# Kernel optimization log

Hardware: AMD Instinct MI355X
Metric: run time of the kernel (lower is better)

The kernel has to match this reference:

```python
import jax, jax.numpy as jnp
import numpy as np

N = 16_777_216  # number of draft tokens / cache slots
ACCEPT_PROB = 0.7


def setup_inputs() -> dict:
    key = jax.random.key(0)
    k1, k2, k3 = jax.random.split(key, 3)
    idx = jax.random.randint(k1, (N,), 0, N, dtype=jnp.int64)
    keep = jax.random.uniform(k2, (N,)) < ACCEPT_PROB
    # rejected slots are marked -1, as in the original kernel
    accept_index = jnp.where(keep, idx, jnp.int64(-1))
    out_cache_loc = jax.random.normal(k3, (N,), dtype=jnp.float32)
    return {"accept_index": accept_index, "out_cache_loc": out_cache_loc}


def reference(accept_index, out_cache_loc):
    """Stream compaction: gather out_cache_loc[accept_index[i]] for every i with
    accept_index[i] >= 0, packed densely at the front of the output.

    The original returns an array of length num_accepted (data-dependent). For a
    static, jit-compatible shape we return a length-N array whose first
    num_accepted entries equal the original output and the rest are zero.
    """
    n = accept_index.shape[0]
    mask = accept_index >= 0                      # [N] bool
    # exclusive prefix sum of mask = destination slot for each accepted element
    dst = jnp.cumsum(mask.astype(jnp.int64)) - mask.astype(jnp.int64)  # [N]
    # gather (use 0 as a safe dummy index for rejected lanes)
    vals = out_cache_loc[jnp.where(mask, accept_index, 0)]             # [N]
    # scatter accepted values to their compacted slots; rejected lanes are
    # routed to index n, which mode='drop' discards
    scatter_idx = jnp.where(mask, dst, n)
    out = jnp.zeros((n,), dtype=out_cache_loc.dtype)
    out = out.at[scatter_idx].set(vals, mode="drop")
    return out
```

## Files before the change

kernel.cpp:

```cpp
#include <hip/hip_runtime.h>


#define N_TOTAL  16777216
#define BLOCK    256

#define EPT2     16
#define TILE2    (BLOCK * EPT2)
#define NB2      (N_TOTAL / TILE2)
#define GRID     2048
#define GENS     (NB2 / GRID)

#define SLICE_LG 20
#define SLICES   (N_TOTAL >> SLICE_LG)

typedef float vfloat4 __attribute__((ext_vector_type(4)));
typedef int   vint4   __attribute__((ext_vector_type(4)));

__global__ __launch_bounds__(256) void k_init(unsigned long long* __restrict__ state) {
    state[blockIdx.x * 256 + threadIdx.x] = 0ULL;
}

__global__ __launch_bounds__(BLOCK, 8) void k_compact(const int* __restrict__ idx,
                                                      const float* __restrict__ src,
                                                      float* __restrict__ out,
                                                      unsigned long long* __restrict__ state) {
    const int b = blockIdx.x;
    const int t = threadIdx.x;
    const int lane = t & 63, wave = t >> 6;

    __shared__ int wsum[BLOCK / 64], woff[BLOCK / 64], btotal;
    __shared__ long long sBase;
    __shared__ float vals[TILE2];

    for (int gen = 0; gen < GENS; ++gen) {
        const int tile = b + gen * GRID;

        const vint4* p = (const vint4*)(idx + (size_t)tile * TILE2 + (size_t)t * EPT2);
        int v[EPT2];
#pragma unroll
        for (int j = 0; j < EPT2 / 4; ++j) {
            vint4 q = __builtin_nontemporal_load(p + j);
            v[4 * j + 0] = q.x; v[4 * j + 1] = q.y;
            v[4 * j + 2] = q.z; v[4 * j + 3] = q.w;
        }
        int cnt = 0;
#pragma unroll
        for (int j = 0; j < EPT2; ++j) cnt += (v[j] >= 0);

        int x = cnt;
#pragma unroll
        for (int d = 1; d < 64; d <<= 1) {
            int y = __shfl_up(x, d);
            if (lane >= d) x += y;
        }
        if (lane == 63) wsum[wave] = x;
        __syncthreads();
        if (t == 0) {
            int s = 0;
#pragma unroll
            for (int w = 0; w < BLOCK / 64; ++w) { woff[w] = s; s += wsum[w]; }
            btotal = s;
            if (tile == 0) {
                __hip_atomic_store(&state[0], ((unsigned long long)s << 2) | 2ULL,
                                   __ATOMIC_RELAXED, __HIP_MEMORY_SCOPE_AGENT);
                sBase = 0;
            } else {
                __hip_atomic_store(&state[tile], ((unsigned long long)s << 2) | 1ULL,
                                   __ATOMIC_RELAXED, __HIP_MEMORY_SCOPE_AGENT);
            }
        }
        __syncthreads();

        const int off0 = (x - cnt) + woff[wave];

#pragma unroll 1
        for (int s = 0; s < SLICES; ++s) {
            float tmp[EPT2];
#pragma unroll
            for (int j = 0; j < EPT2; ++j) {
                const bool m = (int)((unsigned)v[j] >> SLICE_LG) == s;
                tmp[j] = src[m ? v[j] : 0];
            }
            asm volatile("s_waitcnt vmcnt(0)" ::: "memory");
            int o = off0;
#pragma unroll
            for (int j = 0; j < EPT2; ++j) {
                const bool acc = v[j] >= 0;
                const bool m = (int)((unsigned)v[j] >> SLICE_LG) == s;
                if (m) vals[o] = tmp[j];
                o += acc;
            }
        }

        if (tile > 0 && wave == 0) {
            long long excl = 0;
            int look = tile - 1;
            for (;;) {
                const int pos = look - lane;
                unsigned long long s = 2ULL;
                if (pos >= 0)
                    s = __hip_atomic_load(&state[pos], __ATOMIC_RELAXED,
                                          __HIP_MEMORY_SCOPE_AGENT);
                for (;;) {
                    const bool need = (pos >= 0) && ((s & 3ULL) == 0ULL);
                    if (!__any(need)) break;
                    if (need) {
                        __builtin_amdgcn_s_sleep(2);
                        s = __hip_atomic_load(&state[pos], __ATOMIC_RELAXED,
                                              __HIP_MEMORY_SCOPE_AGENT);
                    }
                }
                const unsigned long long ball = __ballot((s & 3ULL) == 2ULL);
                const int fp = ball ? (__ffsll((long long)ball) - 1) : 64;
                long long c = (lane <= fp) ? (long long)(s >> 2) : 0;
#pragma unroll
                for (int d = 32; d; d >>= 1) c += __shfl_down(c, d);
                excl += __shfl(c, 0);
                if (ball) break;
                look -= 64;
            }
            if (lane == 0) {
                __hip_atomic_store(&state[tile],
                                   (((unsigned long long)(excl + btotal)) << 2) | 2ULL,
                                   __ATOMIC_RELAXED, __HIP_MEMORY_SCOPE_AGENT);
                sBase = excl;
            }
        }
        __syncthreads();

        const int tot = btotal;
        const long long base = sBase;

        {
            const long long gbeg = base, gend = base + tot;
            const long long a0 = (gbeg + 3) & ~3LL;
            const long long a1 = gend & ~3LL;
            const long long hend = a0 < gend ? a0 : gend;
            for (long long g = gbeg + t; g < hend; g += BLOCK)
                __builtin_nontemporal_store(vals[(int)(g - gbeg)], out + g);
            if (a0 < gend) {
                for (long long g = a0 + (long long)t * 4; g < a1; g += (long long)BLOCK * 4) {
                    const int l = (int)(g - gbeg);
                    vfloat4 w = { vals[l], vals[l + 1], vals[l + 2], vals[l + 3] };
                    __builtin_nontemporal_store(w, (vfloat4*)(out + g));
                }
                for (long long g = a1 + t; g < gend; g += BLOCK)
                    __builtin_nontemporal_store(vals[(int)(g - gbeg)], out + g);
            }
        }

        {
            const long long rprev = (long long)tile * TILE2 - base;
            const int rcnt = TILE2 - tot;
            const long long zbeg = (long long)N_TOTAL - rprev - rcnt;
            const long long zend = (long long)N_TOTAL - rprev;
            const long long a0 = (zbeg + 3) & ~3LL;
            const long long a1 = zend & ~3LL;
            const long long hend = a0 < zend ? a0 : zend;
            for (long long g = zbeg + t; g < hend; g += BLOCK)
                __builtin_nontemporal_store(0.0f, out + g);
            if (a0 < zend) {
                const vfloat4 z = (vfloat4)(0.f);
                for (long long g = a0 + (long long)t * 4; g < a1; g += (long long)BLOCK * 4)
                    __builtin_nontemporal_store(z, (vfloat4*)(out + g));
                for (long long g = a1 + t; g < zend; g += BLOCK)
                    __builtin_nontemporal_store(0.0f, out + g);
            }
        }

        __syncthreads();
    }
}

extern "C" void kernel_launch(void* const* d_in, const int* in_sizes, int n_in,
                              void* d_out, int out_size, void* d_ws, size_t ws_size,
                              hipStream_t stream) {
    const int*   idx = (const int*)d_in[0];
    const float* src = (const float*)d_in[1];
    float*       out = (float*)d_out;

    unsigned long long* state = (unsigned long long*)d_ws;

    k_init   <<<NB2 / 256, 256, 0, stream>>>(state);
    k_compact<<<GRID, BLOCK, 0, stream>>>(idx, src, out, state);
}
```

Measured before the change: 328.3 us.

## Double-buffer sliced gathers and launch one block per tile

Drops the persistent generation loop: the kernel now launches one block per tile (NB2 blocks) and lowers the launch-bounds occupancy hint from 8 to 4. The per-slice gather is software-pipelined with two register buffers, so one slice's loads are issued before the previous slice is committed to LDS, waiting on vmcnt(16) instead of draining to zero. Gathers now use nontemporal loads, and masked-out lanes point at the start of the current slice instead of index 0. The aim is to hide gather latency and remove the per-generation barrier overhead. The cost is higher register pressure, possible loss of L2 reuse from the nontemporal hint, and a decoupled look-back that now relies on in-order block dispatch across many more blocks.

```diff
diff --git a/kernel.cpp b/kernel.cpp
--- a/kernel.cpp
+++ b/kernel.cpp
@@ -7,9 +7,6 @@
 #define EPT2     16
 #define TILE2    (BLOCK * EPT2)
 #define NB2      (N_TOTAL / TILE2)
-#define GRID     2048
-#define GENS     (NB2 / GRID)
-
 #define SLICE_LG 20
 #define SLICES   (N_TOTAL >> SLICE_LG)
 
@@ -20,7 +17,27 @@
     state[blockIdx.x * 256 + threadIdx.x] = 0ULL;
 }
 
-__global__ __launch_bounds__(BLOCK, 8) void k_compact(const int* __restrict__ idx,
+#define GATHER_ISSUE(sl, tmp)                                              \
+    _Pragma("unroll")                                                      \
+    for (int j = 0; j < EPT2; ++j) {                                       \
+        const bool m_ = (int)((unsigned)v[j] >> SLICE_LG) == (sl);         \
+        const int a_ = m_ ? v[j] : ((sl) << SLICE_LG);                     \
+        tmp[j] = __builtin_nontemporal_load(src + a_);                     \
+    }
+
+#define GATHER_COMMIT(sl, tmp)                                             \
+    {                                                                      \
+        int o_ = off0;                                                     \
+        _Pragma("unroll")                                                  \
+        for (int j = 0; j < EPT2; ++j) {                                   \
+            const bool acc_ = v[j] >= 0;                                   \
+            const bool m_ = (int)((unsigned)v[j] >> SLICE_LG) == (sl);     \
+            if (m_) vals[o_] = tmp[j];                                     \
+            o_ += acc_;                                                    \
+        }                                                                  \
+    }
+
+__global__ __launch_bounds__(BLOCK, 4) void k_compact(const int* __restrict__ idx,
                                                       const float* __restrict__ src,
                                                       float* __restrict__ out,
                                                       unsigned long long* __restrict__ state) {
@@ -32,143 +49,136 @@
     __shared__ long long sBase;
     __shared__ float vals[TILE2];
 
-    for (int gen = 0; gen < GENS; ++gen) {
-        const int tile = b + gen * GRID;
+    const vint4* p = (const vint4*)(idx + (size_t)b * TILE2 + (size_t)t * EPT2);
+    int v[EPT2];
+#pragma unroll
+    for (int j = 0; j < EPT2 / 4; ++j) {
+        vint4 q = __builtin_nontemporal_load(p + j);
+        v[4 * j + 0] = q.x; v[4 * j + 1] = q.y;
+        v[4 * j + 2] = q.z; v[4 * j + 3] = q.w;
+    }
+    int cnt = 0;
+#pragma unroll
+    for (int j = 0; j < EPT2; ++j) cnt += (v[j] >= 0);
 
-        const vint4* p = (const vint4*)(idx + (size_t)tile * TILE2 + (size_t)t * EPT2);
-        int v[EPT2];
+    int x = cnt;
 #pragma unroll
-        for (int j = 0; j < EPT2 / 4; ++j) {
-            vint4 q = __builtin_nontemporal_load(p + j);
-            v[4 * j + 0] = q.x; v[4 * j + 1] = q.y;
-            v[4 * j + 2] = q.z; v[4 * j + 3] = q.w;
+    for (int d = 1; d < 64; d <<= 1) {
+        int y = __shfl_up(x, d);
+        if (lane >= d) x += y;
+    }
+    if (lane == 63) wsum[wave] = x;
+    __syncthreads();
+    if (t == 0) {
+        int s = 0;
+#pragma unroll
+        for (int w = 0; w < BLOCK / 64; ++w) { woff[w] = s; s += wsum[w]; }
+        btotal = s;
+        if (b == 0) {
+            __hip_atomic_store(&state[0], ((unsigned long long)s << 2) | 2ULL,
+                               __ATOMIC_RELAXED, __HIP_MEMORY_SCOPE_AGENT);
+            sBase = 0;
+        } else {
+            __hip_atomic_store(&state[b], ((unsigned long long)s << 2) | 1ULL,
+                               __ATOMIC_RELAXED, __HIP_MEMORY_SCOPE_AGENT);
         }
-        int cnt = 0;
-#pragma unroll
-        for (int j = 0; j < EPT2; ++j) cnt += (v[j] >= 0);
+    }
+    __syncthreads();
 
-        int x = cnt;
-#pragma unroll
-        for (int d = 1; d < 64; d <<= 1) {
-            int y = __shfl_up(x, d);
-            if (lane >= d) x += y;
+    const int off0 = (x - cnt) + woff[wave];
+
+    {
+        float tA[EPT2], tB[EPT2];
+        GATHER_ISSUE(0, tA);
+#pragma unroll 1
+        for (int s = 0; s < SLICES; s += 2) {
+            GATHER_ISSUE(s + 1, tB);
+            asm volatile("s_waitcnt vmcnt(16)" ::: "memory");
+            GATHER_COMMIT(s, tA);
+            if (s + 2 < SLICES) {
+                GATHER_ISSUE(s + 2, tA);
+                asm volatile("s_waitcnt vmcnt(16)" ::: "memory");
+            } else {
+                asm volatile("s_waitcnt vmcnt(0)" ::: "memory");
+            }
+            GATHER_COMMIT(s + 1, tB);
         }
-        if (lane == 63) wsum[wave] = x;
-        __syncthreads();
-        if (t == 0) {
-            int s = 0;
-#pragma unroll
-            for (int w = 0; w < BLOCK / 64; ++w) { woff[w] = s; s += wsum[w]; }
-            btotal = s;
-            if (tile == 0) {
-                __hip_atomic_store(&state[0], ((unsigned long long)s << 2) | 2ULL,
-                                   __ATOMIC_RELAXED, __HIP_MEMORY_SCOPE_AGENT);
-                sBase = 0;
-            } else {
-                __hip_atomic_store(&state[tile], ((unsigned long long)s << 2) | 1ULL,
-                                   __ATOMIC_RELAXED, __HIP_MEMORY_SCOPE_AGENT);
-            }
-        }
-        __syncthreads();
+    }
 
-        const int off0 = (x - cnt) + woff[wave];
-
-#pragma unroll 1
-        for (int s = 0; s < SLICES; ++s) {
-            float tmp[EPT2];
-#pragma unroll
-            for (int j = 0; j < EPT2; ++j) {
-                const bool m = (int)((unsigned)v[j] >> SLICE_LG) == s;
-                tmp[j] = src[m ? v[j] : 0];
-            }
-            asm volatile("s_waitcnt vmcnt(0)" ::: "memory");
-            int o = off0;
-#pragma unroll
-            for (int j = 0; j < EPT2; ++j) {
-                const bool acc = v[j] >= 0;
-                const bool m = (int)((unsigned)v[j] >> SLICE_LG) == s;
-                if (m) vals[o] = tmp[j];
-                o += acc;
-            }
-        }
-
-        if (tile > 0 && wave == 0) {
-            long long excl = 0;
-            int look = tile - 1;
+    if (b > 0 && wave == 0) {
+        long long excl = 0;
+        int look = b - 1;
+        for (;;) {
+            const int pos = look - lane;
+            unsigned long long s = 2ULL;
+            if (pos >= 0)
+                s = __hip_atomic_load(&state[pos], __ATOMIC_RELAXED,
+                                      __HIP_MEMORY_SCOPE_AGENT);
             for (;;) {
-                const int pos = look - lane;
-                unsigned long long s = 2ULL;
-                if (pos >= 0)
+                const bool need = (pos >= 0) && ((s & 3ULL) == 0ULL);
+                if (!__any(need)) break;
+                if (need) {
+                    __builtin_amdgcn_s_sleep(2);
                     s = __hip_atomic_load(&state[pos], __ATOMIC_RELAXED,
                                           __HIP_MEMORY_SCOPE_AGENT);
-                for (;;) {
-                    const bool need = (pos >= 0) && ((s & 3ULL) == 0ULL);
-                    if (!__any(need)) break;
-                    if (need) {
-                        __builtin_amdgcn_s_sleep(2);
-                        s = __hip_atomic_load(&state[pos], __ATOMIC_RELAXED,
-                                              __HIP_MEMORY_SCOPE_AGENT);
-                    }
                 }
-                const unsigned long long ball = __ballot((s & 3ULL) == 2ULL);
-                const int fp = ball ? (__ffsll((long long)ball) - 1) : 64;
-                long long c = (lane <= fp) ? (long long)(s >> 2) : 0;
+            }
+            const unsigned long long ball = __ballot((s & 3ULL) == 2ULL);
+            const int fp = ball ? (__ffsll((long long)ball) - 1) : 64;
+            long long c = (lane <= fp) ? (long long)(s >> 2) : 0;
 #pragma unroll
-                for (int d = 32; d; d >>= 1) c += __shfl_down(c, d);
-                excl += __shfl(c, 0);
-                if (ball) break;
-                look -= 64;
+            for (int d = 32; d; d >>= 1) c += __shfl_down(c, d);
+            excl += __shfl(c, 0);
+            if (ball) break;
+            look -= 64;
+        }
+        if (lane == 0) {
+            __hip_atomic_store(&state[b],
+                               (((unsigned long long)(excl + btotal)) << 2) | 2ULL,
+                               __ATOMIC_RELAXED, __HIP_MEMORY_SCOPE_AGENT);
+            sBase = excl;
+        }
+    }
+    __syncthreads();
+
+    const int tot = btotal;
+    const long long base = sBase;
+
+    {
+        const long long gbeg = base, gend = base + tot;
+        const long long a0 = (gbeg + 3) & ~3LL;
+        const long long a1 = gend & ~3LL;
+        const long long hend = a0 < gend ? a0 : gend;
+        for (long long g = gbeg + t; g < hend; g += BLOCK)
+            __builtin_nontemporal_store(vals[(int)(g - gbeg)], out + g);
+        if (a0 < gend) {
+            for (long long g = a0 + (long long)t * 4; g < a1; g += (long long)BLOCK * 4) {
+                const int l = (int)(g - gbeg);
+                vfloat4 w = { vals[l], vals[l + 1], vals[l + 2], vals[l + 3] };
+                __builtin_nontemporal_store(w, (vfloat4*)(out + g));
             }
-            if (lane == 0) {
-                __hip_atomic_store(&state[tile],
-                                   (((unsigned long long)(excl + btotal)) << 2) | 2ULL,
-                                   __ATOMIC_RELAXED, __HIP_MEMORY_SCOPE_AGENT);
-                sBase = excl;
-            }
+            for (long long g = a1 + t; g < gend; g += BLOCK)
+                __builtin_nontemporal_store(vals[(int)(g - gbeg)], out + g);
         }
-        __syncthreads();
+    }
 
-        const int tot = btotal;
-        const long long base = sBase;
-
-        {
-            const long long gbeg = base, gend = base + tot;
-            const long long a0 = (gbeg + 3) & ~3LL;
-            const long long a1 = gend & ~3LL;
-            const long long hend = a0 < gend ? a0 : gend;
-            for (long long g = gbeg + t; g < hend; g += BLOCK)
-                __builtin_nontemporal_store(vals[(int)(g - gbeg)], out + g);
-            if (a0 < gend) {
-                for (long long g = a0 + (long long)t * 4; g < a1; g += (long long)BLOCK * 4) {
-                    const int l = (int)(g - gbeg);
-                    vfloat4 w = { vals[l], vals[l + 1], vals[l + 2], vals[l + 3] };
-                    __builtin_nontemporal_store(w, (vfloat4*)(out + g));
-                }
-                for (long long g = a1 + t; g < gend; g += BLOCK)
-                    __builtin_nontemporal_store(vals[(int)(g - gbeg)], out + g);
-            }
+    {
+        const long long rprev = (long long)b * TILE2 - base;
+        const int rcnt = TILE2 - tot;
+        const long long zbeg = (long long)N_TOTAL - rprev - rcnt;
+        const long long zend = (long long)N_TOTAL - rprev;
+        const long long a0 = (zbeg + 3) & ~3LL;
+        const long long a1 = zend & ~3LL;
+        const long long hend = a0 < zend ? a0 : zend;
+        for (long long g = zbeg + t; g < hend; g += BLOCK)
+            __builtin_nontemporal_store(0.0f, out + g);
+        if (a0 < zend) {
+            const vfloat4 z = (vfloat4)(0.f);
+            for (long long g = a0 + (long long)t * 4; g < a1; g += (long long)BLOCK * 4)
+                __builtin_nontemporal_store(z, (vfloat4*)(out + g));
+            for (long long g = a1 + t; g < zend; g += BLOCK)
+                __builtin_nontemporal_store(0.0f, out + g);
         }
-
-        {
-            const long long rprev = (long long)tile * TILE2 - base;
-            const int rcnt = TILE2 - tot;
-            const long long zbeg = (long long)N_TOTAL - rprev - rcnt;
-            const long long zend = (long long)N_TOTAL - rprev;
-            const long long a0 = (zbeg + 3) & ~3LL;
-            const long long a1 = zend & ~3LL;
-            const long long hend = a0 < zend ? a0 : zend;
-            for (long long g = zbeg + t; g < hend; g += BLOCK)
-                __builtin_nontemporal_store(0.0f, out + g);
-            if (a0 < zend) {
-                const vfloat4 z = (vfloat4)(0.f);
-                for (long long g = a0 + (long long)t * 4; g < a1; g += (long long)BLOCK * 4)
-                    __builtin_nontemporal_store(z, (vfloat4*)(out + g));
-                for (long long g = a1 + t; g < zend; g += BLOCK)
-                    __builtin_nontemporal_store(0.0f, out + g);
-            }
-        }
-
-        __syncthreads();
     }
 }
 
@@ -182,5 +192,5 @@
     unsigned long long* state = (unsigned long long*)d_ws;
 
     k_init   <<<NB2 / 256, 256, 0, stream>>>(state);
-    k_compact<<<GRID, BLOCK, 0, stream>>>(idx, src, out, state);
+    k_compact<<<NB2, BLOCK, 0, stream>>>(idx, src, out, state);
 }
```

Measured after the change: 447.0 us. 36.2% more time.

## Bin accepted indices by source region before gathering to improve cache locality

Applied to the files above, without the earlier changes.

Replaces the single-pass compaction, which swept all source slices per tile, with a multi-kernel pipeline. It histograms accepted indices into 64 source regions, scans the counts, and bins (destination, index) pairs by region into workspace. It then gathers per region with XCD-aware block mapping so each region's source stays cache-resident, and writes the output in 32K-element chunks staged through LDS. The aim is to remove the 16x redundant slice gather loads and the random-access misses, at the cost of extra workspace traffic (dst/val arrays written and read several times) and more kernel launches. A fallback path keeps the old single-kernel approach when the workspace is too small.

```diff
diff --git a/kernel.cpp b/kernel.cpp
--- a/kernel.cpp
+++ b/kernel.cpp
@@ -3,16 +3,29 @@
 
 #define N_TOTAL  16777216
 #define BLOCK    256
-
-#define EPT2     16
-#define TILE2    (BLOCK * EPT2)
-#define NB2      (N_TOTAL / TILE2)
-#define GRID     2048
-#define GENS     (NB2 / GRID)
+#define EPT      16
+#define TILE     (BLOCK * EPT)
+#define NB       (N_TOTAL / TILE)
+
+#define NR       64
+#define REG_LG   18
+#define CSTR     4100
+
+#define CHUNK_LG 15
+#define CHUNK    (1 << CHUNK_LG)
+#define NCH      (N_TOTAL / CHUNK)
 
 #define SLICE_LG 20
 #define SLICES   (N_TOTAL >> SLICE_LG)
 
+#define OFF_STATE 0ull
+#define OFF_DST   32768ull
+#define OFF_VAL   (OFF_DST + 4ull * N_TOTAL)
+#define OFF_BB    (OFF_VAL + 4ull * N_TOTAL)
+#define OFF_CNT   (OFF_BB + 16400ull)
+#define OFF_RB    (OFF_CNT + 4ull * NR * CSTR)
+#define WS_NEED   (OFF_RB + 4ull * (NR + 1))
+
 typedef float vfloat4 __attribute__((ext_vector_type(4)));
 typedef int   vint4   __attribute__((ext_vector_type(4)));
 
@@ -20,155 +33,471 @@
     state[blockIdx.x * 256 + threadIdx.x] = 0ULL;
 }
 
-__global__ __launch_bounds__(BLOCK, 8) void k_compact(const int* __restrict__ idx,
-                                                      const float* __restrict__ src,
-                                                      float* __restrict__ out,
-                                                      unsigned long long* __restrict__ state) {
+__global__ __launch_bounds__(BLOCK) void k_histA(const int* __restrict__ idx,
+                                                 unsigned long long* __restrict__ state,
+                                                 int* __restrict__ blockBase,
+                                                 int* __restrict__ cntArr) {
     const int b = blockIdx.x;
     const int t = threadIdx.x;
     const int lane = t & 63, wave = t >> 6;
 
+    __shared__ int hist[NR];
     __shared__ int wsum[BLOCK / 64], woff[BLOCK / 64], btotal;
     __shared__ long long sBase;
-    __shared__ float vals[TILE2];
-
-    for (int gen = 0; gen < GENS; ++gen) {
-        const int tile = b + gen * GRID;
-
-        const vint4* p = (const vint4*)(idx + (size_t)tile * TILE2 + (size_t)t * EPT2);
-        int v[EPT2];
-#pragma unroll
-        for (int j = 0; j < EPT2 / 4; ++j) {
-            vint4 q = __builtin_nontemporal_load(p + j);
-            v[4 * j + 0] = q.x; v[4 * j + 1] = q.y;
-            v[4 * j + 2] = q.z; v[4 * j + 3] = q.w;
-        }
-        int cnt = 0;
-#pragma unroll
-        for (int j = 0; j < EPT2; ++j) cnt += (v[j] >= 0);
-
-        int x = cnt;
-#pragma unroll
-        for (int d = 1; d < 64; d <<= 1) {
-            int y = __shfl_up(x, d);
-            if (lane >= d) x += y;
-        }
-        if (lane == 63) wsum[wave] = x;
-        __syncthreads();
-        if (t == 0) {
-            int s = 0;
-#pragma unroll
-            for (int w = 0; w < BLOCK / 64; ++w) { woff[w] = s; s += wsum[w]; }
-            btotal = s;
-            if (tile == 0) {
-                __hip_atomic_store(&state[0], ((unsigned long long)s << 2) | 2ULL,
-                                   __ATOMIC_RELAXED, __HIP_MEMORY_SCOPE_AGENT);
-                sBase = 0;
-            } else {
-                __hip_atomic_store(&state[tile], ((unsigned long long)s << 2) | 1ULL,
-                                   __ATOMIC_RELAXED, __HIP_MEMORY_SCOPE_AGENT);
-            }
-        }
-        __syncthreads();
-
-        const int off0 = (x - cnt) + woff[wave];
-
-#pragma unroll 1
-        for (int s = 0; s < SLICES; ++s) {
-            float tmp[EPT2];
-#pragma unroll
-            for (int j = 0; j < EPT2; ++j) {
-                const bool m = (int)((unsigned)v[j] >> SLICE_LG) == s;
-                tmp[j] = src[m ? v[j] : 0];
-            }
-            asm volatile("s_waitcnt vmcnt(0)" ::: "memory");
-            int o = off0;
-#pragma unroll
-            for (int j = 0; j < EPT2; ++j) {
-                const bool acc = v[j] >= 0;
-                const bool m = (int)((unsigned)v[j] >> SLICE_LG) == s;
-                if (m) vals[o] = tmp[j];
-                o += acc;
-            }
-        }
-
-        if (tile > 0 && wave == 0) {
-            long long excl = 0;
-            int look = tile - 1;
+    for (int r = t; r < NR; r += BLOCK) hist[r] = 0;
+
+    const vint4* p = (const vint4*)(idx + (size_t)b * TILE + (size_t)t * EPT);
+    int v[EPT];
+#pragma unroll
+    for (int j = 0; j < EPT / 4; ++j) {
+        vint4 q = __builtin_nontemporal_load(p + j);
+        v[4 * j + 0] = q.x; v[4 * j + 1] = q.y;
+        v[4 * j + 2] = q.z; v[4 * j + 3] = q.w;
+    }
+    int ca = 0;
+#pragma unroll
+    for (int j = 0; j < EPT; ++j) ca += (v[j] >= 0);
+
+    int x = ca;
+#pragma unroll
+    for (int d = 1; d < 64; d <<= 1) {
+        int y = __shfl_up(x, d);
+        if (lane >= d) x += y;
+    }
+    if (lane == 63) wsum[wave] = x;
+    __syncthreads();
+    if (t == 0) {
+        int s = 0;
+#pragma unroll
+        for (int w = 0; w < BLOCK / 64; ++w) { woff[w] = s; s += wsum[w]; }
+        btotal = s;
+        if (b == 0) {
+            __hip_atomic_store(&state[0], ((unsigned long long)s << 2) | 2ULL,
+                               __ATOMIC_RELAXED, __HIP_MEMORY_SCOPE_AGENT);
+            sBase = 0;
+        } else {
+            __hip_atomic_store(&state[b], ((unsigned long long)s << 2) | 1ULL,
+                               __ATOMIC_RELAXED, __HIP_MEMORY_SCOPE_AGENT);
+        }
+    }
+    __syncthreads();
+
+#pragma unroll
+    for (int j = 0; j < EPT; ++j)
+        if (v[j] >= 0) atomicAdd(&hist[v[j] >> REG_LG], 1);
+    __syncthreads();
+    if (t < NR) cntArr[t * CSTR + b] = hist[t];
+
+    if (b > 0 && wave == 0) {
+        long long excl = 0;
+        int look = b - 1;
+        for (;;) {
+            const int pos = look - lane;
+            unsigned long long s = 2ULL;
+            if (pos >= 0)
+                s = __hip_atomic_load(&state[pos], __ATOMIC_RELAXED,
+                                      __HIP_MEMORY_SCOPE_AGENT);
             for (;;) {
-                const int pos = look - lane;
-                unsigned long long s = 2ULL;
-                if (pos >= 0)
+                const bool need = (pos >= 0) && ((s & 3ULL) == 0ULL);
+                if (!__any(need)) break;
+                if (need) {
+                    __builtin_amdgcn_s_sleep(2);
                     s = __hip_atomic_load(&state[pos], __ATOMIC_RELAXED,
                                           __HIP_MEMORY_SCOPE_AGENT);
-                for (;;) {
-                    const bool need = (pos >= 0) && ((s & 3ULL) == 0ULL);
-                    if (!__any(need)) break;
-                    if (need) {
-                        __builtin_amdgcn_s_sleep(2);
-                        s = __hip_atomic_load(&state[pos], __ATOMIC_RELAXED,
-                                              __HIP_MEMORY_SCOPE_AGENT);
-                    }
                 }
-                const unsigned long long ball = __ballot((s & 3ULL) == 2ULL);
-                const int fp = ball ? (__ffsll((long long)ball) - 1) : 64;
-                long long c = (lane <= fp) ? (long long)(s >> 2) : 0;
-#pragma unroll
-                for (int d = 32; d; d >>= 1) c += __shfl_down(c, d);
-                excl += __shfl(c, 0);
-                if (ball) break;
-                look -= 64;
             }
-            if (lane == 0) {
-                __hip_atomic_store(&state[tile],
-                                   (((unsigned long long)(excl + btotal)) << 2) | 2ULL,
-                                   __ATOMIC_RELAXED, __HIP_MEMORY_SCOPE_AGENT);
-                sBase = excl;
+            const unsigned long long ball = __ballot((s & 3ULL) == 2ULL);
+            const int fp = ball ? (__ffsll((long long)ball) - 1) : 64;
+            long long c = (lane <= fp) ? (long long)(s >> 2) : 0;
+#pragma unroll
+            for (int d = 32; d; d >>= 1) c += __shfl_down(c, d);
+            excl += __shfl(c, 0);
+            if (ball) break;
+            look -= 64;
+        }
+        if (lane == 0) {
+            __hip_atomic_store(&state[b],
+                               (((unsigned long long)(excl + btotal)) << 2) | 2ULL,
+                               __ATOMIC_RELAXED, __HIP_MEMORY_SCOPE_AGENT);
+            sBase = excl;
+        }
+    }
+    __syncthreads();
+    if (t == 0) blockBase[b] = (int)(b == 0 ? 0 : sBase);
+}
+
+__global__ __launch_bounds__(256) void k_scan64(int* __restrict__ cntArr) {
+    const int r = blockIdx.x, t = threadIdx.x;
+    const int lane = t & 63, wave = t >> 6;
+    int* row = cntArr + r * CSTR;
+    int vals[16];
+    const vint4* p = (const vint4*)(row + t * 16);
+#pragma unroll
+    for (int j = 0; j < 4; ++j) {
+        vint4 q = p[j];
+        vals[4 * j + 0] = q.x; vals[4 * j + 1] = q.y;
+        vals[4 * j + 2] = q.z; vals[4 * j + 3] = q.w;
+    }
+    int tsum = 0;
+#pragma unroll
+    for (int j = 0; j < 16; ++j) tsum += vals[j];
+    int x = tsum;
+#pragma unroll
+    for (int d = 1; d < 64; d <<= 1) {
+        int y = __shfl_up(x, d);
+        if (lane >= d) x += y;
+    }
+    __shared__ int wsum[4], woff[4];
+    if (lane == 63) wsum[wave] = x;
+    __syncthreads();
+    if (t == 0) {
+        int s = 0;
+#pragma unroll
+        for (int w = 0; w < 4; ++w) { woff[w] = s; s += wsum[w]; }
+        row[4096] = s;
+    }
+    __syncthreads();
+    int run = (x - tsum) + woff[wave];
+#pragma unroll
+    for (int j = 0; j < 16; ++j) {
+        row[t * 16 + j] = run;
+        run += vals[j];
+    }
+}
+
+__global__ __launch_bounds__(64) void k_scan2(const int* __restrict__ cntArr,
+                                              int* __restrict__ regionBase,
+                                              int* __restrict__ blockBase) {
+    const int t = threadIdx.x;
+    int x = cntArr[t * CSTR + 4096];
+    int incl = x;
+#pragma unroll
+    for (int d = 1; d < 64; d <<= 1) {
+        int y = __shfl_up(incl, d);
+        if (t >= d) incl += y;
+    }
+    regionBase[t] = incl - x;
+    if (t == 63) { regionBase[64] = incl; blockBase[4096] = incl; }
+}
+
+__global__ __launch_bounds__(BLOCK) void k_binB(const int* __restrict__ idx,
+                                                const int* __restrict__ blockBase,
+                                                const int* __restrict__ cntArr,
+                                                const int* __restrict__ regionBase,
+                                                int* __restrict__ dstArr,
+                                                int* __restrict__ valArr) {
+    const int b = blockIdx.x;
+    const int t = threadIdx.x;
+    const int lane = t & 63, wave = t >> 6;
+
+    __shared__ int hist[NR], rscan[NR + 1], rcnt[NR], sG[NR];
+    __shared__ int ldsD[TILE], ldsV[TILE];
+    __shared__ int wsum[BLOCK / 64], woff[BLOCK / 64], btotal;
+    for (int r = t; r < NR; r += BLOCK) { hist[r] = 0; rcnt[r] = 0; }
+
+    const vint4* p = (const vint4*)(idx + (size_t)b * TILE + (size_t)t * EPT);
+    int v[EPT];
+#pragma unroll
+    for (int j = 0; j < EPT / 4; ++j) {
+        vint4 q = __builtin_nontemporal_load(p + j);
+        v[4 * j + 0] = q.x; v[4 * j + 1] = q.y;
+        v[4 * j + 2] = q.z; v[4 * j + 3] = q.w;
+    }
+    int ca = 0;
+#pragma unroll
+    for (int j = 0; j < EPT; ++j) ca += (v[j] >= 0);
+
+    int x = ca;
+#pragma unroll
+    for (int d = 1; d < 64; d <<= 1) {
+        int y = __shfl_up(x, d);
+        if (lane >= d) x += y;
+    }
+    if (lane == 63) wsum[wave] = x;
+    __syncthreads();
+    if (t == 0) {
+        int s = 0;
+#pragma unroll
+        for (int w = 0; w < BLOCK / 64; ++w) { woff[w] = s; s += wsum[w]; }
+        btotal = s;
+    }
+    __syncthreads();
+    const int off0 = (x - ca) + woff[wave];
+    const int base = blockBase[b];
+
+#pragma unroll
+    for (int j = 0; j < EPT; ++j)
+        if (v[j] >= 0) atomicAdd(&hist[v[j] >> REG_LG], 1);
+    __syncthreads();
+    if (t == 0) {
+        int s = 0;
+#pragma unroll
+        for (int r = 0; r < NR; ++r) { rscan[r] = s; s += hist[r]; }
+        rscan[NR] = s;
+    }
+    if (t < NR) sG[t] = regionBase[t] + cntArr[t * CSTR + b];
+    __syncthreads();
+
+    int o = off0;
+#pragma unroll
+    for (int j = 0; j < EPT; ++j) {
+        if (v[j] >= 0) {
+            const int r = v[j] >> REG_LG;
+            const int pos = rscan[r] + atomicAdd(&rcnt[r], 1);
+            ldsD[pos] = base + o;
+            ldsV[pos] = v[j];
+            ++o;
+        }
+    }
+    __syncthreads();
+
+    const int tot = btotal;
+    for (int i = t; i < tot; i += BLOCK) {
+        int loR = 0, hiR = NR;
+        while (hiR - loR > 1) {
+            const int mid = (loR + hiR) >> 1;
+            if (rscan[mid] <= i) loR = mid; else hiR = mid;
+        }
+        const int g = sG[loR] + (i - rscan[loR]);
+        dstArr[g] = ldsD[i];
+        valArr[g] = ldsV[i];
+    }
+}
+
+__global__ __launch_bounds__(BLOCK) void k_gather(const float* __restrict__ src,
+                                                  const int* __restrict__ cntArr,
+                                                  const int* __restrict__ regionBase,
+                                                  int* __restrict__ valArr) {
+    const int b = blockIdx.x, t = threadIdx.x;
+    const int xcd = b & 7, w = b >> 3;
+#pragma unroll 1
+    for (int ti = 0; ti < 8; ++ti) {
+        const int r = xcd * 8 + ti;
+        const int tot = cntArr[r * CSTR + 4096];
+        const int rb = regionBase[r];
+        const int per = (tot + 255) >> 8;
+        const int s0 = w * per;
+        const int s1 = (s0 + per < tot) ? s0 + per : tot;
+        int i = s0 + t;
+        for (; i + 3 * BLOCK < s1; i += 4 * BLOCK) {
+            const int a0 = __builtin_nontemporal_load(valArr + rb + i);
+            const int a1 = __builtin_nontemporal_load(valArr + rb + i + BLOCK);
+            const int a2 = __builtin_nontemporal_load(valArr + rb + i + 2 * BLOCK);
+            const int a3 = __builtin_nontemporal_load(valArr + rb + i + 3 * BLOCK);
+            const float f0 = src[a0], f1 = src[a1], f2 = src[a2], f3 = src[a3];
+            __builtin_nontemporal_store(__float_as_int(f0), valArr + rb + i);
+            __builtin_nontemporal_store(__float_as_int(f1), valArr + rb + i + BLOCK);
+            __builtin_nontemporal_store(__float_as_int(f2), valArr + rb + i + 2 * BLOCK);
+            __builtin_nontemporal_store(__float_as_int(f3), valArr + rb + i + 3 * BLOCK);
+        }
+        for (; i < s1; i += BLOCK) {
+            const int a = __builtin_nontemporal_load(valArr + rb + i);
+            __builtin_nontemporal_store(__float_as_int(src[a]), valArr + rb + i);
+        }
+    }
+}
+
+__global__ __launch_bounds__(BLOCK) void k_chunk(const int* __restrict__ blockBase,
+                                                 const int* __restrict__ cntArr,
+                                                 const int* __restrict__ regionBase,
+                                                 const int* __restrict__ dstArr,
+                                                 const int* __restrict__ valArr,
+                                                 float* __restrict__ out) {
+    const int m = blockIdx.x, t = threadIdx.x;
+    const int lo = m << CHUNK_LG, hi = lo + CHUNK;
+    __shared__ int buf[CHUNK];
+    __shared__ int sblo, sbhi;
+    __shared__ int segA[NR], segB[NR], segC[NR], segD[NR];
+
+    for (int i = t * 4; i < CHUNK; i += BLOCK * 4)
+        *(vint4*)(buf + i) = (vint4)(0);
+
+    if (t == 0) {
+        int a = 0, c = NB - 1;
+        while (a < c) { const int mid = (a + c + 1) >> 1;
+                        if (blockBase[mid] <= lo) a = mid; else c = mid - 1; }
+        sblo = a;
+        a = 0; c = NB - 1;
+        while (a < c) { const int mid = (a + c + 1) >> 1;
+                        if (blockBase[mid] < hi) a = mid; else c = mid - 1; }
+        sbhi = a;
+    }
+    __syncthreads();
+    const int blo = sblo, bhi = sbhi;
+    if (t < NR) {
+        segA[t] = regionBase[t] + cntArr[t * CSTR + blo];
+        segB[t] = regionBase[t] + cntArr[t * CSTR + blo + 1];
+        segC[t] = regionBase[t] + cntArr[t * CSTR + bhi];
+        segD[t] = regionBase[t] + cntArr[t * CSTR + bhi + 1];
+    }
+    __syncthreads();
+
+#pragma unroll 1
+    for (int r = 0; r < NR; ++r) {
+        for (int j = segB[r] + t; j < segC[r]; j += BLOCK)
+            buf[__builtin_nontemporal_load(dstArr + j) - lo] =
+                __builtin_nontemporal_load(valArr + j);
+        for (int j = segA[r] + t; j < segB[r]; j += BLOCK) {
+            const int d = __builtin_nontemporal_load(dstArr + j);
+            if (d >= lo && d < hi)
+                buf[d - lo] = __builtin_nontemporal_load(valArr + j);
+        }
+        if (bhi != blo)
+            for (int j = segC[r] + t; j < segD[r]; j += BLOCK) {
+                const int d = __builtin_nontemporal_load(dstArr + j);
+                if (d >= lo && d < hi)
+                    buf[d - lo] = __builtin_nontemporal_load(valArr + j);
             }
-        }
-        __syncthreads();
-
-        const int tot = btotal;
-        const long long base = sBase;
-
-        {
-            const long long gbeg = base, gend = base + tot;
-            const long long a0 = (gbeg + 3) & ~3LL;
-            const long long a1 = gend & ~3LL;
-            const long long hend = a0 < gend ? a0 : gend;
-            for (long long g = gbeg + t; g < hend; g += BLOCK)
+    }
+    __syncthreads();
+
+    for (int i = t * 4; i < CHUNK; i += BLOCK * 4) {
+        vfloat4 q = { __int_as_float(buf[i]), __int_as_float(buf[i + 1]),
+                      __int_as_float(buf[i + 2]), __int_as_float(buf[i + 3]) };
+        __builtin_nontemporal_store(q, (vfloat4*)(out + lo + i));
+    }
+}
+
+__global__ __launch_bounds__(BLOCK, 8) void fb_compact(const int* __restrict__ idx,
+                                                       const float* __restrict__ src,
+                                                       float* __restrict__ out,
+                                                       unsigned long long* __restrict__ state) {
+    const int b = blockIdx.x;
+    const int t = threadIdx.x;
+    const int lane = t & 63, wave = t >> 6;
+
+    __shared__ int wsum[BLOCK / 64], woff[BLOCK / 64], btotal;
+    __shared__ long long sBase;
+    __shared__ float vals[TILE];
+
+    const vint4* p = (const vint4*)(idx + (size_t)b * TILE + (size_t)t * EPT);
+    int v[EPT];
+#pragma unroll
+    for (int j = 0; j < EPT / 4; ++j) {
+        vint4 q = __builtin_nontemporal_load(p + j);
+        v[4 * j + 0] = q.x; v[4 * j + 1] = q.y;
+        v[4 * j + 2] = q.z; v[4 * j + 3] = q.w;
+    }
+    int ca = 0;
+#pragma unroll
+    for (int j = 0; j < EPT; ++j) ca += (v[j] >= 0);
+
+    int x = ca;
+#pragma unroll
+    for (int d = 1; d < 64; d <<= 1) {
+        int y = __shfl_up(x, d);
+        if (lane >= d) x += y;
+    }
+    if (lane == 63) wsum[wave] = x;
+    __syncthreads();
+    if (t == 0) {
+        int s = 0;
+#pragma unroll
+        for (int w = 0; w < BLOCK / 64; ++w) { woff[w] = s; s += wsum[w]; }
+        btotal = s;
+        if (b == 0) {
+            __hip_atomic_store(&state[0], ((unsigned long long)s << 2) | 2ULL,
+                               __ATOMIC_RELAXED, __HIP_MEMORY_SCOPE_AGENT);
+            sBase = 0;
+        } else {
+            __hip_atomic_store(&state[b], ((unsigned long long)s << 2) | 1ULL,
+                               __ATOMIC_RELAXED, __HIP_MEMORY_SCOPE_AGENT);
+        }
+    }
+    __syncthreads();
+
+    const int off0 = (x - ca) + woff[wave];
+#pragma unroll 1
+    for (int s = 0; s < SLICES; ++s) {
+        float tmp[EPT];
+#pragma unroll
+        for (int j = 0; j < EPT; ++j) {
+            const bool m = (int)((unsigned)v[j] >> SLICE_LG) == s;
+            tmp[j] = src[m ? v[j] : 0];
+        }
+        asm volatile("s_waitcnt vmcnt(0)" ::: "memory");
+        int o = off0;
+#pragma unroll
+        for (int j = 0; j < EPT; ++j) {
+            const bool acc = v[j] >= 0;
+            const bool m = (int)((unsigned)v[j] >> SLICE_LG) == s;
+            if (m) vals[o] = tmp[j];
+            o += acc;
+        }
+    }
+
+    if (b > 0 && wave == 0) {
+        long long excl = 0;
+        int look = b - 1;
+        for (;;) {
+            const int pos = look - lane;
+            unsigned long long s = 2ULL;
+            if (pos >= 0)
+                s = __hip_atomic_load(&state[pos], __ATOMIC_RELAXED,
+                                      __HIP_MEMORY_SCOPE_AGENT);
+            for (;;) {
+                const bool need = (pos >= 0) && ((s & 3ULL) == 0ULL);
+                if (!__any(need)) break;
+                if (need) {
+                    __builtin_amdgcn_s_sleep(2);
+                    s = __hip_atomic_load(&state[pos], __ATOMIC_RELAXED,
+                                          __HIP_MEMORY_SCOPE_AGENT);
+                }
+            }
+            const unsigned long long ball = __ballot((s & 3ULL) == 2ULL);
+            const int fp = ball ? (__ffsll((long long)ball) - 1) : 64;
+            long long c = (lane <= fp) ? (long long)(s >> 2) : 0;
+#pragma unroll
+            for (int d = 32; d; d >>= 1) c += __shfl_down(c, d);
+            excl += __shfl(c, 0);
+            if (ball) break;
+            look -= 64;
+        }
+        if (lane == 0) {
+            __hip_atomic_store(&state[b],
+                               (((unsigned long long)(excl + btotal)) << 2) | 2ULL,
+                               __ATOMIC_RELAXED, __HIP_MEMORY_SCOPE_AGENT);
+            sBase = excl;
+        }
+    }
+    __syncthreads();
+
+    const int tot = btotal;
+    const long long base = sBase;
+    {
+        const long long gbeg = base, gend = base + tot;
+        const long long a0 = (gbeg + 3) & ~3LL;
+        const long long a1 = gend & ~3LL;
+        const long long hend = a0 < gend ? a0 : gend;
+        for (long long g = gbeg + t; g < hend; g += BLOCK)
+            __builtin_nontemporal_store(vals[(int)(g - gbeg)], out + g);
+        if (a0 < gend) {
+            for (long long g = a0 + (long long)t * 4; g < a1; g += (long long)BLOCK * 4) {
+                const int l = (int)(g - gbeg);
+                vfloat4 w = { vals[l], vals[l + 1], vals[l + 2], vals[l + 3] };
+                __builtin_nontemporal_store(w, (vfloat4*)(out + g));
+            }
+            for (long long g = a1 + t; g < gend; g += BLOCK)
                 __builtin_nontemporal_store(vals[(int)(g - gbeg)], out + g);
-            if (a0 < gend) {
-                for (long long g = a0 + (long long)t * 4; g < a1; g += (long long)BLOCK * 4) {
-                    const int l = (int)(g - gbeg);
-                    vfloat4 w = { vals[l], vals[l + 1], vals[l + 2], vals[l + 3] };
-                    __builtin_nontemporal_store(w, (vfloat4*)(out + g));
-                }
-                for (long long g = a1 + t; g < gend; g += BLOCK)
-                    __builtin_nontemporal_store(vals[(int)(g - gbeg)], out + g);
-            }
-        }
-
-        {
-            const long long rprev = (long long)tile * TILE2 - base;
-            const int rcnt = TILE2 - tot;
-            const long long zbeg = (long long)N_TOTAL - rprev - rcnt;
-            const long long zend = (long long)N_TOTAL - rprev;
-            const long long a0 = (zbeg + 3) & ~3LL;
-            const long long a1 = zend & ~3LL;
-            const long long hend = a0 < zend ? a0 : zend;
-            for (long long g = zbeg + t; g < hend; g += BLOCK)
+        }
+    }
+    {
+        const long long rprev = (long long)b * TILE - base;
+        const int rcnt2 = TILE - tot;
+        const long long zbeg = (long long)N_TOTAL - rprev - rcnt2;
+        const long long zend = (long long)N_TOTAL - rprev;
+        const long long a0 = (zbeg + 3) & ~3LL;
+        const long long a1 = zend & ~3LL;
+        const long long hend = a0 < zend ? a0 : zend;
+        for (long long g = zbeg + t; g < hend; g += BLOCK)
+            __builtin_nontemporal_store(0.0f, out + g);
+        if (a0 < zend) {
+            const vfloat4 z = (vfloat4)(0.f);
+            for (long long g = a0 + (long long)t * 4; g < a1; g += (long long)BLOCK * 4)
+                __builtin_nontemporal_store(z, (vfloat4*)(out + g));
+            for (long long g = a1 + t; g < zend; g += BLOCK)
                 __builtin_nontemporal_store(0.0f, out + g);
-            if (a0 < zend) {
-                const vfloat4 z = (vfloat4)(0.f);
-                for (long long g = a0 + (long long)t * 4; g < a1; g += (long long)BLOCK * 4)
-                    __builtin_nontemporal_store(z, (vfloat4*)(out + g));
-                for (long long g = a1 + t; g < zend; g += BLOCK)
-                    __builtin_nontemporal_store(0.0f, out + g);
-            }
-        }
-
-        __syncthreads();
+        }
     }
 }
 
@@ -179,8 +508,27 @@
     const float* src = (const float*)d_in[1];
     float*       out = (float*)d_out;
 
-    unsigned long long* state = (unsigned long long*)d_ws;
-
-    k_init   <<<NB2 / 256, 256, 0, stream>>>(state);
-    k_compact<<<GRID, BLOCK, 0, stream>>>(idx, src, out, state);
-}
+    char* w = (char*)d_ws;
+    unsigned long long* state = (unsigned long long*)(w + OFF_STATE);
+
+    if (ws_size >= WS_NEED) {
+        int* dstArr     = (int*)(w + OFF_DST);
+        int* valArr     = (int*)(w + OFF_VAL);
+        int* blockBase  = (int*)(w + OFF_BB);
+        int* cntArr     = (int*)(w + OFF_CNT);
+        int* regionBase = (int*)(w + OFF_RB);
+
+        k_init  <<<16, 256, 0, stream>>>(state);
+        k_histA <<<NB, BLOCK, 0, stream>>>(idx, state, blockBase, cntArr);
+        k_scan64<<<NR, 256, 0, stream>>>(cntArr);
+        k_scan2 <<<1, 64, 0, stream>>>(cntArr, regionBase, blockBase);
+        k_binB  <<<NB, BLOCK, 0, stream>>>(idx, blockBase, cntArr, regionBase,
+                                           dstArr, valArr);
+        k_gather<<<2048, BLOCK, 0, stream>>>(src, cntArr, regionBase, valArr);
+        k_chunk <<<NCH, BLOCK, 0, stream>>>(blockBase, cntArr, regionBase,
+                                            dstArr, valArr, out);
+    } else {
+        k_init    <<<16, 256, 0, stream>>>(state);
+        fb_compact<<<NB, BLOCK, 0, stream>>>(idx, src, out, state);
+    }
+}
```

Measured after the change: 681.0 us. +107.4%, slower.
